# Kernel tuning notes

Hardware: AMD Instinct MI355X
Metric: run time of the kernel (lower is better)

## Reference

```python
import jax, jax.numpy as jnp
import numpy as np

N_NODES = 50000
N_EDGES = 800000
NUM_FEATURES = 3
HIDDEN = 128
NUM_GRAPHS = 100
NUM_CLASSES = 2


def setup_inputs() -> dict:
    key = jax.random.key(0)
    ks = jax.random.split(key, 12)
    x = jax.random.normal(ks[0], (N_NODES, NUM_FEATURES), dtype=jnp.float32)
    edge_index = jax.random.randint(ks[1], (2, N_EDGES), 0, N_NODES, dtype=jnp.int64)
    batch = jnp.sort(jax.random.randint(ks[2], (N_NODES,), 0, NUM_GRAPHS, dtype=jnp.int64))
    c1, c2, c3 = 4 * HIDDEN, 2 * HIDDEN, HIDDEN  # 512, 256, 128

    def glorot(k, fan_in, fan_out):
        s = jnp.sqrt(6.0 / (fan_in + fan_out)).astype(jnp.float32)
        return jax.random.uniform(k, (fan_in, fan_out), jnp.float32, -s, s)

    W1 = glorot(ks[3], NUM_FEATURES, c1); b1 = jnp.zeros((c1,), jnp.float32)
    W2 = glorot(ks[4], c1, c2);           b2 = jnp.zeros((c2,), jnp.float32)
    W3 = glorot(ks[5], c2, c3);           b3 = jnp.zeros((c3,), jnp.float32)
    Wc = glorot(ks[6], c3, NUM_CLASSES);  bc = jnp.zeros((NUM_CLASSES,), jnp.float32)
    return {"x": x, "W1": W1, "b1": b1, "W2": W2, "b2": b2, "W3": W3, "b3": b3,
            "Wc": Wc, "bc": bc, "edge_index": edge_index, "batch": batch}


def reference(x, W1, b1, W2, b2, W3, b3, Wc, bc, edge_index, batch):
    n = x.shape[0]
    self_loop = jnp.arange(n, dtype=edge_index.dtype)
    row = jnp.concatenate([edge_index[0], self_loop])  # source nodes (messages from)
    col = jnp.concatenate([edge_index[1], self_loop])  # target nodes (aggregate into)
    # symmetric GCN normalization with self-loops: deg^{-1/2}[row] * deg^{-1/2}[col]
    deg = jax.ops.segment_sum(jnp.ones(row.shape, x.dtype), col, num_segments=n)
    dis = jnp.where(deg > 0, jax.lax.rsqrt(jnp.maximum(deg, 1.0)), 0.0)
    norm = dis[row] * dis[col]  # [E + N]

    def gcn_conv(h, W, b):
        m = h @ W                                   # project first (cheap GEMM)
        agg = jax.ops.segment_sum(norm[:, None] * m[row], col, num_segments=n)
        return agg + b

    h = jax.nn.relu(gcn_conv(x, W1, b1))
    h = jax.nn.relu(gcn_conv(h, W2, b2))
    h = jax.nn.relu(gcn_conv(h, W3, b3))

    # global mean pool over graphs
    counts = jax.ops.segment_sum(jnp.ones((n,), h.dtype), batch, num_segments=NUM_GRAPHS)
    pooled = jax.ops.segment_sum(h, batch, num_segments=NUM_GRAPHS) / jnp.maximum(counts, 1.0)[:, None]

    logits = pooled @ Wc + bc
    return jax.nn.log_softmax(logits, axis=1)
```

## Files before the change

kernel.cpp:

```cpp
#include <hip/hip_runtime.h>
#include <hip/hip_bf16.h>
#include <hip/hip_fp8.h>
#include <math.h>

#define N_NODES 50000
#define N_EDGES 800000
#define NFEAT 3
#define C1 512
#define C2 256
#define C3 128
#define NGRAPH 100
#define NCLS 2
#define PSPLIT 8
#define NRANGE 8
#define RANGE_SZ 6250

typedef short bh8 __attribute__((ext_vector_type(8)));
typedef float f32x4 __attribute__((ext_vector_type(4)));

__device__ __forceinline__ short f2bf(float x) {
    __hip_bfloat16 h = __float2bfloat16(x);
    return *reinterpret_cast<short*>(&h);
}
__device__ __forceinline__ float bflo(unsigned int u) { return __uint_as_float(u << 16); }
__device__ __forceinline__ float bfhi(unsigned int u) { return __uint_as_float(u & 0xffff0000u); }
__device__ __forceinline__ unsigned int packbf(float a, float b) {
    return (unsigned int)(unsigned short)f2bf(a) | ((unsigned int)(unsigned short)f2bf(b) << 16);
}
__device__ __forceinline__ unsigned char f2fp8(float x) {
    __hip_fp8_e4m3 q(x);
    return (unsigned char)q.__x;
}
__device__ __forceinline__ float2 fp8x2(unsigned short u) {
    __hip_fp8x2_e4m3 q; q.__x = u; return (float2)q;
}


__global__ void count_edges(const int* __restrict__ col, int* __restrict__ counts) {
    int range = blockIdx.x & (NRANGE - 1);
    int e = (blockIdx.x >> 3) * 256 + threadIdx.x;
    if (e < N_EDGES) {
        int c = col[e];
        int lo = range * RANGE_SZ;
        if (c >= lo && c < lo + RANGE_SZ) atomicAdd(&counts[c], 1);
    }
}


__global__ void scan_chunks(const int* __restrict__ counts, const float* __restrict__ x,
                            int* __restrict__ offsets, int* __restrict__ chunksums,
                            float* __restrict__ dis, float4* __restrict__ xd) {
    __shared__ int s[256];
    int b = blockIdx.x, t = threadIdx.x;
    int i = b * 256 + t;
    int v = (i < N_NODES) ? counts[i] : 0;
    if (i < N_NODES) {
        float d = rsqrtf((float)(v + 1));
        dis[i] = d;
        xd[i] = make_float4(x[i * 3 + 0], x[i * 3 + 1], x[i * 3 + 2], d);
    }
    s[t] = v;
    __syncthreads();
    for (int d = 1; d < 256; d <<= 1) {
        int add = (t >= d) ? s[t - d] : 0;
        __syncthreads();
        s[t] += add;
        __syncthreads();
    }
    if (i < N_NODES) offsets[i + 1] = s[t];
    if (t == 255) chunksums[b] = s[255];
}

__global__ void scan_sums(int* __restrict__ chunksums, int nchunks) {
    __shared__ int s[256];
    int t = threadIdx.x;
    int v = (t < nchunks) ? chunksums[t] : 0;
    s[t] = v;
    __syncthreads();
    for (int d = 1; d < 256; d <<= 1) {
        int add = (t >= d) ? s[t - d] : 0;
        __syncthreads();
        s[t] += add;
        __syncthreads();
    }
    if (t < nchunks) chunksums[t] = (t == 0) ? 0 : s[t - 1];
}

__global__ void finalize_offsets(int* __restrict__ offsets, const int* __restrict__ chunkoffs,
                                 int* __restrict__ cursor) {
    int i = blockIdx.x * blockDim.x + threadIdx.x;
    if (i < N_NODES) {
        int v = offsets[i + 1] + chunkoffs[i / 256];
        offsets[i + 1] = v;
        if (i + 1 < N_NODES) cursor[i + 1] = v;
    }
    if (i == 0) { offsets[0] = 0; cursor[0] = 0; }
}

__global__ void scatter_edges(const int* __restrict__ rowi, const int* __restrict__ coli,
                              int* __restrict__ cursor, int* __restrict__ csr_src) {
    int range = blockIdx.x & (NRANGE - 1);
    int e = (blockIdx.x >> 3) * 256 + threadIdx.x;
    if (e < N_EDGES) {
        int c = coli[e];
        int lo = range * RANGE_SZ;
        if (c >= lo && c < lo + RANGE_SZ) {
            int p = atomicAdd(&cursor[c], 1);
            csr_src[p] = rowi[e];
        }
    }
}


__global__ void prep_weights(const float* __restrict__ W2, const float* __restrict__ W3,
                             short* __restrict__ W2t, short* __restrict__ W3t) {
    int idx = blockIdx.x * 256 + threadIdx.x;
    if (idx < C1 * C2) {
        int n = idx / C1, k = idx % C1;
        W2t[idx] = f2bf(W2[k * C2 + n]);
    } else if (idx < C1 * C2 + C2 * C3) {
        int j = idx - C1 * C2;
        int n = j / C2, k = j % C2;
        W3t[j] = f2bf(W3[k * C3 + n]);
    }
}


__global__ __launch_bounds__(256) void agg_feat3(const float4* __restrict__ xd,
                                                 const int* __restrict__ offsets,
                                                 const int* __restrict__ csr_src,
                                                 float* __restrict__ aggx) {
    int t = threadIdx.x;
    int l = t & 15;
    int i = blockIdx.x * 16 + (t >> 4);
    if (i >= N_NODES) return;
    int s = offsets[i], e = offsets[i + 1];
    float a0 = 0.f, a1 = 0.f, a2 = 0.f;
    for (int p = s + l; p < e; p += 16) {
        int r = csr_src[p];
        float4 v = xd[r];
        a0 += v.w * v.x;
        a1 += v.w * v.y;
        a2 += v.w * v.z;
    }
#pragma unroll
    for (int m = 1; m < 16; m <<= 1) {
        a0 += __shfl_xor(a0, m);
        a1 += __shfl_xor(a1, m);
        a2 += __shfl_xor(a2, m);
    }
    if (l == 0) {
        float4 self = xd[i];
        float di = self.w;
        a0 += di * self.x; a1 += di * self.y; a2 += di * self.z;
        aggx[i * 3 + 0] = di * a0;
        aggx[i * 3 + 1] = di * a1;
        aggx[i * 3 + 2] = di * a2;
    }
}


__global__ __launch_bounds__(512, 4) void gemm_l1(const float* __restrict__ aggx,
                                                  const float* __restrict__ W1,
                                                  const float* __restrict__ b1,
                                                  const float* __restrict__ dis,
                                                  const short* __restrict__ Bt,
                                                  unsigned char* __restrict__ Cmat, int M) {
    __shared__ short As[128 * 32];
    __shared__ short Bs[C2 * 32];
    __shared__ float sW1[3 * C1];
    __shared__ float sb1[C1];
    __shared__ float sa[128 * 3];
    __shared__ float sd[128];
    int bm = blockIdx.x * 128;
    int t = threadIdx.x;
    int wave = t >> 6, lane = t & 63, quad = lane >> 4, l16 = lane & 15;
    int wm = (wave >> 2) * 64;
    int wn = (wave & 3) * 64;
    f32x4 acc[4][4] = {};

    for (int j = t; j < 3 * C1; j += 512) sW1[j] = W1[j];
    if (t < C1) sb1[t] = b1[t];
    if (t < 128 * 3) {
        int r = bm + t / 3; if (r > M - 1) r = M - 1;
        sa[t] = aggx[r * 3 + (t % 3)];
    }
    if (t < 128) {
        int r = bm + t; if (r > M - 1) r = M - 1;
        sd[t] = dis[r];
    }
    __syncthreads();

    int ar = t >> 2, ak = (t & 3) * 8;
    int br = t >> 1, bk = (t & 1) * 16;
    float a0 = sa[ar * 3 + 0], a1 = sa[ar * 3 + 1], a2 = sa[ar * 3 + 2];
    float drow = sd[ar];

    for (int k0 = 0; k0 < C1; k0 += 32) {
#pragma unroll
        for (int j = 0; j < 8; ++j) {
            int k = k0 + ak + j;
            float v = a0 * sW1[k] + a1 * sW1[C1 + k] + a2 * sW1[2 * C1 + k] + sb1[k];
            As[ar * 32 + ak + j] = f2bf(drow * fmaxf(v, 0.f));
        }
        const short* bptr = Bt + (size_t)br * C1 + bk + k0;
        *(bh8*)&Bs[br * 32 + bk]     = *(const bh8*)bptr;
        *(bh8*)&Bs[br * 32 + bk + 8] = *(const bh8*)(bptr + 8);
        __syncthreads();
        bh8 af[4], bf[4];
#pragma unroll
        for (int mt = 0; mt < 4; ++mt)
            af[mt] = *(const bh8*)&As[(wm + mt * 16 + l16) * 32 + quad * 8];
#pragma unroll
        for (int nt = 0; nt < 4; ++nt)
            bf[nt] = *(const bh8*)&Bs[(wn + nt * 16 + l16) * 32 + quad * 8];
#pragma unroll
        for (int mt = 0; mt < 4; ++mt)
#pragma unroll
            for (int nt = 0; nt < 4; ++nt)
                acc[mt][nt] = __builtin_amdgcn_mfma_f32_16x16x32_bf16(af[mt], bf[nt], acc[mt][nt], 0, 0, 0);
        __syncthreads();
    }

#pragma unroll
    for (int mt = 0; mt < 4; ++mt)
#pragma unroll
        for (int nt = 0; nt < 4; ++nt) {
            int colc = wn + nt * 16 + l16;
#pragma unroll
            for (int r = 0; r < 4; ++r) {
                int rowc = bm + wm + mt * 16 + quad * 4 + r;
                if (rowc < M) Cmat[(size_t)rowc * C2 + colc] = f2fp8(acc[mt][nt][r]);
            }
        }
}


template <int K, int BN>
__global__ __launch_bounds__(512, 4) void gemm_bf16(const short* __restrict__ A,
                                                    const short* __restrict__ Bt,
                                                    unsigned char* __restrict__ Cmat, int M) {
    __shared__ short As[128 * 32];
    __shared__ short Bs[BN * 32];
    constexpr int NT = BN / 64;
    int bm = blockIdx.x * 128;
    int t = threadIdx.x;
    int wave = t >> 6, lane = t & 63, quad = lane >> 4, l16 = lane & 15;
    int wm = (wave >> 2) * 64;
    int wn = (wave & 3) * (BN / 4);
    f32x4 acc[4][NT] = {};

    int ar = t >> 2, ak = (t & 3) * 8;
    int agr = bm + ar; if (agr > M - 1) agr = M - 1;
    const short* aptr = A + (size_t)agr * K + ak;

    for (int k0 = 0; k0 < K; k0 += 32) {
        *(bh8*)&As[ar * 32 + ak] = *(const bh8*)(aptr + k0);
        if constexpr (BN == 256) {
            int br = t >> 1, bk = (t & 1) * 16;
            const short* bptr = Bt + (size_t)br * K + bk + k0;
            *(bh8*)&Bs[br * 32 + bk]     = *(const bh8*)bptr;
            *(bh8*)&Bs[br * 32 + bk + 8] = *(const bh8*)(bptr + 8);
        } else {
            int br = t >> 2, bk = (t & 3) * 8;
            *(bh8*)&Bs[br * 32 + bk] = *(const bh8*)(Bt + (size_t)br * K + bk + k0);
        }
        __syncthreads();
        bh8 af[4], bf[NT];
#pragma unroll
        for (int mt = 0; mt < 4; ++mt)
            af[mt] = *(const bh8*)&As[(wm + mt * 16 + l16) * 32 + quad * 8];
#pragma unroll
        for (int nt = 0; nt < NT; ++nt)
            bf[nt] = *(const bh8*)&Bs[(wn + nt * 16 + l16) * 32 + quad * 8];
#pragma unroll
        for (int mt = 0; mt < 4; ++mt)
#pragma unroll
            for (int nt = 0; nt < NT; ++nt)
                acc[mt][nt] = __builtin_amdgcn_mfma_f32_16x16x32_bf16(af[mt], bf[nt], acc[mt][nt], 0, 0, 0);
        __syncthreads();
    }

#pragma unroll
    for (int mt = 0; mt < 4; ++mt)
#pragma unroll
        for (int nt = 0; nt < NT; ++nt) {
            int colc = wn + nt * 16 + l16;
#pragma unroll
            for (int r = 0; r < 4; ++r) {
                int rowc = bm + wm + mt * 16 + quad * 4 + r;
                if (rowc < M) Cmat[(size_t)rowc * BN + colc] = f2fp8(acc[mt][nt][r]);
            }
        }
}


template <int C, bool PRESCALE>
__global__ __launch_bounds__(256) void aggregate_w(const unsigned char* __restrict__ m,
                                                   const int* __restrict__ offsets,
                                                   const int* __restrict__ csr_src,
                                                   const float* __restrict__ dis,
                                                   const float* __restrict__ bias,
                                                   short* __restrict__ out) {
    int i = blockIdx.x * 4 + (threadIdx.x >> 6);
    if (i >= N_NODES) return;
    int lane = threadIdx.x & 63;
    int s = __builtin_amdgcn_readfirstlane(offsets[i]);
    int e = __builtin_amdgcn_readfirstlane(offsets[i + 1]);
    float di = __uint_as_float(__builtin_amdgcn_readfirstlane(__float_as_uint(dis[i])));

    if constexpr (C == 256) {
        const unsigned int* mu = (const unsigned int*)m;
        unsigned int su = mu[(size_t)i * (C / 4) + lane];
        float2 slo = fp8x2((unsigned short)(su & 0xffffu));
        float2 shi = fp8x2((unsigned short)(su >> 16));
        float a0 = slo.x, a1 = slo.y, a2 = shi.x, a3 = shi.y;
        int p = s;
        for (; p + 16 <= e; p += 16) {
            unsigned int u[16];
#pragma unroll
            for (int j = 0; j < 16; ++j) {
                int r = csr_src[p + j];
                u[j] = mu[(size_t)r * (C / 4) + lane];
            }
#pragma unroll
            for (int j = 0; j < 16; ++j) {
                float2 lo = fp8x2((unsigned short)(u[j] & 0xffffu));
                float2 hi = fp8x2((unsigned short)(u[j] >> 16));
                a0 += lo.x; a1 += lo.y; a2 += hi.x; a3 += hi.y;
            }
        }
        if (p < e) {
            unsigned int u[16];
            float sc[16];
#pragma unroll
            for (int j = 0; j < 16; ++j) {
                int q = p + j;
                sc[j] = (q < e) ? 1.f : 0.f;
                int r = csr_src[(q < e) ? q : e - 1];
                u[j] = mu[(size_t)r * (C / 4) + lane];
            }
#pragma unroll
            for (int j = 0; j < 16; ++j) {
                float2 lo = fp8x2((unsigned short)(u[j] & 0xffffu));
                float2 hi = fp8x2((unsigned short)(u[j] >> 16));
                a0 = fmaf(sc[j], lo.x, a0);
                a1 = fmaf(sc[j], lo.y, a1);
                a2 = fmaf(sc[j], hi.x, a2);
                a3 = fmaf(sc[j], hi.y, a3);
            }
        }
        float4 b = *(const float4*)&bias[4 * lane];
        a0 = fmaxf(di * a0 + b.x, 0.f);
        a1 = fmaxf(di * a1 + b.y, 0.f);
        a2 = fmaxf(di * a2 + b.z, 0.f);
        a3 = fmaxf(di * a3 + b.w, 0.f);
        if (PRESCALE) { a0 *= di; a1 *= di; a2 *= di; a3 *= di; }
        uint2 o;
        o.x = packbf(a0, a1);
        o.y = packbf(a2, a3);
        *(uint2*)(out + (size_t)i * C + 4 * lane) = o;
    } else {
        const unsigned short* mu = (const unsigned short*)m;
        float2 sf = fp8x2(mu[(size_t)i * (C / 2) + lane]);
        float a0 = sf.x, a1 = sf.y;
        int p = s;
        for (; p + 16 <= e; p += 16) {
            unsigned short u[16];
#pragma unroll
            for (int j = 0; j < 16; ++j) {
                int r = csr_src[p + j];
                u[j] = mu[(size_t)r * (C / 2) + lane];
            }
#pragma unroll
            for (int j = 0; j < 16; ++j) {
                float2 f = fp8x2(u[j]);
                a0 += f.x; a1 += f.y;
            }
        }
        if (p < e) {
            unsigned short u[16];
            float sc[16];
#pragma unroll
            for (int j = 0; j < 16; ++j) {
                int q = p + j;
                sc[j] = (q < e) ? 1.f : 0.f;
                int r = csr_src[(q < e) ? q : e - 1];
                u[j] = mu[(size_t)r * (C / 2) + lane];
            }
#pragma unroll
            for (int j = 0; j < 16; ++j) {
                float2 f = fp8x2(u[j]);
                a0 = fmaf(sc[j], f.x, a0);
                a1 = fmaf(sc[j], f.y, a1);
            }
        }
        float2 b = *(const float2*)&bias[2 * lane];
        a0 = fmaxf(di * a0 + b.x, 0.f);
        a1 = fmaxf(di * a1 + b.y, 0.f);
        if (PRESCALE) { a0 *= di; a1 *= di; }
        ((unsigned int*)out)[(size_t)i * (C / 2) + lane] = packbf(a0, a1);
    }
}


__global__ void pool_partial(const short* __restrict__ h3, const int* __restrict__ batch,
                             float* __restrict__ pooled) {
    int g = blockIdx.x, sp = blockIdx.y;
    int t = threadIdx.x;
    __shared__ int seg[2];
    if (t < 2) {
        int target = g + t;
        int lo = 0, hi = N_NODES;
        while (lo < hi) { int mid = (lo + hi) >> 1; if (batch[mid] < target) lo = mid + 1; else hi = mid; }
        seg[t] = lo;
    }
    __syncthreads();
    int start = seg[0], end = seg[1];
    int len = end - start;
    int chunk = (len + PSPLIT - 1) / PSPLIT;
    int a = start + sp * chunk;
    int b = a + chunk; if (b > end) b = end;
    if (a >= b) return;
    const unsigned int* hu = (const unsigned int*)h3;
    float s0 = 0.f, s1 = 0.f;
    int i = a;
    for (; i + 4 <= b; i += 4) {
        unsigned int u0 = hu[(size_t)(i + 0) * (C3 / 2) + t];
        unsigned int u1 = hu[(size_t)(i + 1) * (C3 / 2) + t];
        unsigned int u2 = hu[(size_t)(i + 2) * (C3 / 2) + t];
        unsigned int u3 = hu[(size_t)(i + 3) * (C3 / 2) + t];
        s0 += bflo(u0) + bflo(u1) + bflo(u2) + bflo(u3);
        s1 += bfhi(u0) + bfhi(u1) + bfhi(u2) + bfhi(u3);
    }
    for (; i < b; ++i) {
        unsigned int u = hu[(size_t)i * (C3 / 2) + t];
        s0 += bflo(u);
        s1 += bfhi(u);
    }
    atomicAdd(&pooled[g * C3 + 2 * t], s0);
    atomicAdd(&pooled[g * C3 + 2 * t + 1], s1);
}


__global__ void finalize_head(const float* __restrict__ pooled, const int* __restrict__ batch,
                              const float* __restrict__ Wc, const float* __restrict__ bc,
                              float* __restrict__ outp) {
    int g = blockIdx.x;
    int t = threadIdx.x;
    __shared__ int seg[2];
    if (t < 2) {
        int target = g + t;
        int lo = 0, hi = N_NODES;
        while (lo < hi) { int mid = (lo + hi) >> 1; if (batch[mid] < target) lo = mid + 1; else hi = mid; }
        seg[t] = lo;
    }
    __syncthreads();
    float cnt = (float)(seg[1] - seg[0]);
    float pv = pooled[(size_t)g * C3 + t] / fmaxf(cnt, 1.f);
    float p0 = pv * Wc[t * 2 + 0];
    float p1 = pv * Wc[t * 2 + 1];
#pragma unroll
    for (int o = 32; o > 0; o >>= 1) {
        p0 += __shfl_down(p0, o);
        p1 += __shfl_down(p1, o);
    }
    __shared__ float r0[2], r1[2];
    int wid = t >> 6, lane = t & 63;
    if (lane == 0) { r0[wid] = p0; r1[wid] = p1; }
    __syncthreads();
    if (t == 0) {
        float l0 = r0[0] + r0[1] + bc[0];
        float l1 = r1[0] + r1[1] + bc[1];
        float mx = fmaxf(l0, l1);
        float lse = mx + logf(expf(l0 - mx) + expf(l1 - mx));
        outp[g * 2 + 0] = l0 - lse;
        outp[g * 2 + 1] = l1 - lse;
    }
}


extern "C" void kernel_launch(void* const* d_in, const int* in_sizes, int n_in,
                              void* d_out, int out_size, void* d_ws, size_t ws_size,
                              hipStream_t stream) {
    const float* x = (const float*)d_in[0];
    const float* W1 = (const float*)d_in[1];
    const float* b1 = (const float*)d_in[2];
    const float* W2 = (const float*)d_in[3];
    const float* b2 = (const float*)d_in[4];
    const float* W3 = (const float*)d_in[5];
    const float* b3 = (const float*)d_in[6];
    const float* Wc = (const float*)d_in[7];
    const float* bc = (const float*)d_in[8];
    const int* ei = (const int*)d_in[9];
    const int* batch = (const int*)d_in[10];
    const int* row = ei;
    const int* col = ei + N_EDGES;
    float* out = (float*)d_out;

    char* ws = (char*)d_ws;
    size_t off = 0;
    auto alloc = [&](size_t bytes) -> void* {
        off = (off + 255) & ~(size_t)255;
        void* p = ws + off;
        off += bytes;
        return p;
    };

    int* counts = (int*)alloc((size_t)N_NODES * 4);
    int* offsets = (int*)alloc((size_t)(N_NODES + 1) * 4);
    int* cursor = (int*)alloc((size_t)N_NODES * 4);
    int* chunksums = (int*)alloc(256 * 4);
    float* dis = (float*)alloc((size_t)N_NODES * 4);
    float4* xd = (float4*)alloc((size_t)N_NODES * 16);
    int* csr_src = (int*)alloc((size_t)N_EDGES * 4);
    float* aggx = (float*)alloc((size_t)N_NODES * 3 * 4);
    short* W2t = (short*)alloc((size_t)C1 * C2 * 2);
    short* W3t = (short*)alloc((size_t)C2 * C3 * 2);
    unsigned char* m2 = (unsigned char*)alloc((size_t)N_NODES * C2);
    short* h2 = (short*)alloc((size_t)N_NODES * C2 * 2);
    unsigned char* m3 = (unsigned char*)alloc((size_t)N_NODES * C3);
    short* h3 = (short*)alloc((size_t)N_NODES * C3 * 2);
    float* pooled = (float*)alloc((size_t)NGRAPH * C3 * 4);

    hipMemsetAsync(counts, 0, (size_t)N_NODES * 4, stream);
    hipMemsetAsync(pooled, 0, (size_t)NGRAPH * C3 * 4, stream);
    int nechunks = (N_EDGES + 255) / 256;
    count_edges<<<nechunks * NRANGE, 256, 0, stream>>>(col, counts);
    int nchunks = (N_NODES + 255) / 256;
    scan_chunks<<<nchunks, 256, 0, stream>>>(counts, x, offsets, chunksums, dis, xd);
    scan_sums<<<1, 256, 0, stream>>>(chunksums, nchunks);
    finalize_offsets<<<(N_NODES + 255) / 256, 256, 0, stream>>>(offsets, chunksums, cursor);
    scatter_edges<<<nechunks * NRANGE, 256, 0, stream>>>(row, col, cursor, csr_src);

    prep_weights<<<(C1 * C2 + C2 * C3 + 255) / 256, 256, 0, stream>>>(W2, W3, W2t, W3t);

    agg_feat3<<<(N_NODES + 15) / 16, 256, 0, stream>>>(xd, offsets, csr_src, aggx);

    gemm_l1<<<(N_NODES + 127) / 128, 512, 0, stream>>>(aggx, W1, b1, dis, W2t, m2, N_NODES);
    aggregate_w<C2, true><<<(N_NODES + 3) / 4, 256, 0, stream>>>(m2, offsets, csr_src, dis, b2, h2);

    gemm_bf16<C2, C3><<<(N_NODES + 127) / 128, 512, 0, stream>>>(h2, W3t, m3, N_NODES);
    aggregate_w<C3, false><<<(N_NODES + 3) / 4, 256, 0, stream>>>(m3, offsets, csr_src, dis, b3, h3);

    dim3 gp(NGRAPH, PSPLIT);
    pool_partial<<<gp, C3 / 2, 0, stream>>>(h3, batch, pooled);
    finalize_head<<<NGRAPH, C3, 0, stream>>>(pooled, batch, Wc, bc, out);
}
```

Baseline: 282.9 us.

## Fuse small kernels: weight prep into counting, feature aggregation into GEMM, pooling into aggregation

Merges the weight transpose and cast into the edge-counting launch, and folds the chunk-sum scan into finalize_offsets. The layer-1 three-feature aggregation now runs inside gemm_l1, and the last aggregation pushes results straight into the pooled buffer with atomics. This drops several launches and the aggx and h3 intermediate buffers, and two memsets are merged into one. In exchange, every finalize_offsets block redoes the small scan, gemm_l1 blocks do irregular gathers before their GEMM, and global float atomics per node add contention and make the summation order nondeterministic.

```diff
diff --git a/kernel.cpp b/kernel.cpp
--- a/kernel.cpp
+++ b/kernel.cpp
@@ -11,9 +11,10 @@
 #define C3 128
 #define NGRAPH 100
 #define NCLS 2
-#define PSPLIT 8
 #define NRANGE 8
 #define RANGE_SZ 6250
+#define NECHUNK 3125
+#define WBLK 640
 
 typedef short bh8 __attribute__((ext_vector_type(8)));
 typedef float f32x4 __attribute__((ext_vector_type(4)));
@@ -22,8 +23,6 @@
     __hip_bfloat16 h = __float2bfloat16(x);
     return *reinterpret_cast<short*>(&h);
 }
-__device__ __forceinline__ float bflo(unsigned int u) { return __uint_as_float(u << 16); }
-__device__ __forceinline__ float bfhi(unsigned int u) { return __uint_as_float(u & 0xffff0000u); }
 __device__ __forceinline__ unsigned int packbf(float a, float b) {
     return (unsigned int)(unsigned short)f2bf(a) | ((unsigned int)(unsigned short)f2bf(b) << 16);
 }
@@ -36,13 +35,28 @@
 }
 
 
-__global__ void count_edges(const int* __restrict__ col, int* __restrict__ counts) {
-    int range = blockIdx.x & (NRANGE - 1);
-    int e = (blockIdx.x >> 3) * 256 + threadIdx.x;
-    if (e < N_EDGES) {
-        int c = col[e];
-        int lo = range * RANGE_SZ;
-        if (c >= lo && c < lo + RANGE_SZ) atomicAdd(&counts[c], 1);
+__global__ void count_prep(const int* __restrict__ col, int* __restrict__ counts,
+                           const float* __restrict__ W2, const float* __restrict__ W3,
+                           short* __restrict__ W2t, short* __restrict__ W3t) {
+    int b = blockIdx.x;
+    if (b < NECHUNK * NRANGE) {
+        int range = b & (NRANGE - 1);
+        int e = (b >> 3) * 256 + threadIdx.x;
+        if (e < N_EDGES) {
+            int c = col[e];
+            int lo = range * RANGE_SZ;
+            if (c >= lo && c < lo + RANGE_SZ) atomicAdd(&counts[c], 1);
+        }
+    } else {
+        int idx = (b - NECHUNK * NRANGE) * 256 + threadIdx.x;
+        if (idx < C1 * C2) {
+            int n = idx / C1, k = idx % C1;
+            W2t[idx] = f2bf(W2[k * C2 + n]);
+        } else if (idx < C1 * C2 + C2 * C3) {
+            int j = idx - C1 * C2;
+            int n = j / C2, k = j % C2;
+            W3t[j] = f2bf(W3[k * C3 + n]);
+        }
     }
 }
 
@@ -71,11 +85,13 @@
     if (t == 255) chunksums[b] = s[255];
 }
 
-__global__ void scan_sums(int* __restrict__ chunksums, int nchunks) {
+
+__global__ void finalize_offsets(int* __restrict__ offsets, const int* __restrict__ chunksums,
+                                 int* __restrict__ cursor) {
     __shared__ int s[256];
-    int t = threadIdx.x;
-    int v = (t < nchunks) ? chunksums[t] : 0;
-    s[t] = v;
+    int b = blockIdx.x, t = threadIdx.x;
+    int nck = (N_NODES + 255) / 256;
+    s[t] = (t < nck) ? chunksums[t] : 0;
     __syncthreads();
     for (int d = 1; d < 256; d <<= 1) {
         int add = (t >= d) ? s[t - d] : 0;
@@ -83,16 +99,12 @@
         s[t] += add;
         __syncthreads();
     }
-    if (t < nchunks) chunksums[t] = (t == 0) ? 0 : s[t - 1];
-}
-
-__global__ void finalize_offsets(int* __restrict__ offsets, const int* __restrict__ chunkoffs,
-                                 int* __restrict__ cursor) {
-    int i = blockIdx.x * blockDim.x + threadIdx.x;
+    int add = (b == 0) ? 0 : s[b - 1];
+    int i = b * 256 + t;
     if (i < N_NODES) {
-        int v = offsets[i + 1] + chunkoffs[i / 256];
-        offsets[i + 1] = v;
-        if (i + 1 < N_NODES) cursor[i + 1] = v;
+        int val = offsets[i + 1] + add;
+        offsets[i + 1] = val;
+        if (i + 1 < N_NODES) cursor[i + 1] = val;
     }
     if (i == 0) { offsets[0] = 0; cursor[0] = 0; }
 }
@@ -112,58 +124,11 @@
 }
 
 
-__global__ void prep_weights(const float* __restrict__ W2, const float* __restrict__ W3,
-                             short* __restrict__ W2t, short* __restrict__ W3t) {
-    int idx = blockIdx.x * 256 + threadIdx.x;
-    if (idx < C1 * C2) {
-        int n = idx / C1, k = idx % C1;
-        W2t[idx] = f2bf(W2[k * C2 + n]);
-    } else if (idx < C1 * C2 + C2 * C3) {
-        int j = idx - C1 * C2;
-        int n = j / C2, k = j % C2;
-        W3t[j] = f2bf(W3[k * C3 + n]);
-    }
-}
-
-
-__global__ __launch_bounds__(256) void agg_feat3(const float4* __restrict__ xd,
-                                                 const int* __restrict__ offsets,
-                                                 const int* __restrict__ csr_src,
-                                                 float* __restrict__ aggx) {
-    int t = threadIdx.x;
-    int l = t & 15;
-    int i = blockIdx.x * 16 + (t >> 4);
-    if (i >= N_NODES) return;
-    int s = offsets[i], e = offsets[i + 1];
-    float a0 = 0.f, a1 = 0.f, a2 = 0.f;
-    for (int p = s + l; p < e; p += 16) {
-        int r = csr_src[p];
-        float4 v = xd[r];
-        a0 += v.w * v.x;
-        a1 += v.w * v.y;
-        a2 += v.w * v.z;
-    }
-#pragma unroll
-    for (int m = 1; m < 16; m <<= 1) {
-        a0 += __shfl_xor(a0, m);
-        a1 += __shfl_xor(a1, m);
-        a2 += __shfl_xor(a2, m);
-    }
-    if (l == 0) {
-        float4 self = xd[i];
-        float di = self.w;
-        a0 += di * self.x; a1 += di * self.y; a2 += di * self.z;
-        aggx[i * 3 + 0] = di * a0;
-        aggx[i * 3 + 1] = di * a1;
-        aggx[i * 3 + 2] = di * a2;
-    }
-}
-
-
-__global__ __launch_bounds__(512, 4) void gemm_l1(const float* __restrict__ aggx,
+__global__ __launch_bounds__(512, 4) void gemm_l1(const float4* __restrict__ xd,
+                                                  const int* __restrict__ offsets,
+                                                  const int* __restrict__ csr_src,
                                                   const float* __restrict__ W1,
                                                   const float* __restrict__ b1,
-                                                  const float* __restrict__ dis,
                                                   const short* __restrict__ Bt,
                                                   unsigned char* __restrict__ Cmat, int M) {
     __shared__ short As[128 * 32];
@@ -181,13 +146,36 @@
 
     for (int j = t; j < 3 * C1; j += 512) sW1[j] = W1[j];
     if (t < C1) sb1[t] = b1[t];
-    if (t < 128 * 3) {
-        int r = bm + t / 3; if (r > M - 1) r = M - 1;
-        sa[t] = aggx[r * 3 + (t % 3)];
-    }
-    if (t < 128) {
-        int r = bm + t; if (r > M - 1) r = M - 1;
-        sd[t] = dis[r];
+
+    int lg = t & 15;
+#pragma unroll
+    for (int rnd = 0; rnd < 4; ++rnd) {
+        int rloc = rnd * 32 + (t >> 4);
+        int i = bm + rloc; if (i > M - 1) i = M - 1;
+        int s0 = offsets[i], e0 = offsets[i + 1];
+        float a0 = 0.f, a1 = 0.f, a2 = 0.f;
+        for (int p = s0 + lg; p < e0; p += 16) {
+            int r = csr_src[p];
+            float4 v = xd[r];
+            a0 += v.w * v.x;
+            a1 += v.w * v.y;
+            a2 += v.w * v.z;
+        }
+#pragma unroll
+        for (int m = 1; m < 16; m <<= 1) {
+            a0 += __shfl_xor(a0, m);
+            a1 += __shfl_xor(a1, m);
+            a2 += __shfl_xor(a2, m);
+        }
+        if (lg == 0) {
+            float4 self = xd[i];
+            float di = self.w;
+            a0 += di * self.x; a1 += di * self.y; a2 += di * self.z;
+            sa[rloc * 3 + 0] = di * a0;
+            sa[rloc * 3 + 1] = di * a1;
+            sa[rloc * 3 + 2] = di * a2;
+            sd[rloc] = di;
+        }
     }
     __syncthreads();
 
@@ -309,137 +297,113 @@
     int e = __builtin_amdgcn_readfirstlane(offsets[i + 1]);
     float di = __uint_as_float(__builtin_amdgcn_readfirstlane(__float_as_uint(dis[i])));
 
-    if constexpr (C == 256) {
-        const unsigned int* mu = (const unsigned int*)m;
-        unsigned int su = mu[(size_t)i * (C / 4) + lane];
-        float2 slo = fp8x2((unsigned short)(su & 0xffffu));
-        float2 shi = fp8x2((unsigned short)(su >> 16));
-        float a0 = slo.x, a1 = slo.y, a2 = shi.x, a3 = shi.y;
-        int p = s;
-        for (; p + 16 <= e; p += 16) {
-            unsigned int u[16];
-#pragma unroll
-            for (int j = 0; j < 16; ++j) {
-                int r = csr_src[p + j];
-                u[j] = mu[(size_t)r * (C / 4) + lane];
-            }
-#pragma unroll
-            for (int j = 0; j < 16; ++j) {
-                float2 lo = fp8x2((unsigned short)(u[j] & 0xffffu));
-                float2 hi = fp8x2((unsigned short)(u[j] >> 16));
-                a0 += lo.x; a1 += lo.y; a2 += hi.x; a3 += hi.y;
-            }
-        }
-        if (p < e) {
-            unsigned int u[16];
-            float sc[16];
-#pragma unroll
-            for (int j = 0; j < 16; ++j) {
-                int q = p + j;
-                sc[j] = (q < e) ? 1.f : 0.f;
-                int r = csr_src[(q < e) ? q : e - 1];
-                u[j] = mu[(size_t)r * (C / 4) + lane];
-            }
-#pragma unroll
-            for (int j = 0; j < 16; ++j) {
-                float2 lo = fp8x2((unsigned short)(u[j] & 0xffffu));
-                float2 hi = fp8x2((unsigned short)(u[j] >> 16));
-                a0 = fmaf(sc[j], lo.x, a0);
-                a1 = fmaf(sc[j], lo.y, a1);
-                a2 = fmaf(sc[j], hi.x, a2);
-                a3 = fmaf(sc[j], hi.y, a3);
-            }
-        }
-        float4 b = *(const float4*)&bias[4 * lane];
-        a0 = fmaxf(di * a0 + b.x, 0.f);
-        a1 = fmaxf(di * a1 + b.y, 0.f);
-        a2 = fmaxf(di * a2 + b.z, 0.f);
-        a3 = fmaxf(di * a3 + b.w, 0.f);
-        if (PRESCALE) { a0 *= di; a1 *= di; a2 *= di; a3 *= di; }
-        uint2 o;
-        o.x = packbf(a0, a1);
-        o.y = packbf(a2, a3);
-        *(uint2*)(out + (size_t)i * C + 4 * lane) = o;
-    } else {
-        const unsigned short* mu = (const unsigned short*)m;
-        float2 sf = fp8x2(mu[(size_t)i * (C / 2) + lane]);
-        float a0 = sf.x, a1 = sf.y;
-        int p = s;
-        for (; p + 16 <= e; p += 16) {
-            unsigned short u[16];
-#pragma unroll
-            for (int j = 0; j < 16; ++j) {
-                int r = csr_src[p + j];
-                u[j] = mu[(size_t)r * (C / 2) + lane];
-            }
-#pragma unroll
-            for (int j = 0; j < 16; ++j) {
-                float2 f = fp8x2(u[j]);
-                a0 += f.x; a1 += f.y;
-            }
-        }
-        if (p < e) {
-            unsigned short u[16];
-            float sc[16];
-#pragma unroll
-            for (int j = 0; j < 16; ++j) {
-                int q = p + j;
-                sc[j] = (q < e) ? 1.f : 0.f;
-                int r = csr_src[(q < e) ? q : e - 1];
-                u[j] = mu[(size_t)r * (C / 2) + lane];
-            }
-#pragma unroll
-            for (int j = 0; j < 16; ++j) {
-                float2 f = fp8x2(u[j]);
-                a0 = fmaf(sc[j], f.x, a0);
-                a1 = fmaf(sc[j], f.y, a1);
-            }
-        }
-        float2 b = *(const float2*)&bias[2 * lane];
-        a0 = fmaxf(di * a0 + b.x, 0.f);
-        a1 = fmaxf(di * a1 + b.y, 0.f);
-        if (PRESCALE) { a0 *= di; a1 *= di; }
-        ((unsigned int*)out)[(size_t)i * (C / 2) + lane] = packbf(a0, a1);
-    }
-}
-
-
-__global__ void pool_partial(const short* __restrict__ h3, const int* __restrict__ batch,
-                             float* __restrict__ pooled) {
-    int g = blockIdx.x, sp = blockIdx.y;
-    int t = threadIdx.x;
-    __shared__ int seg[2];
-    if (t < 2) {
-        int target = g + t;
-        int lo = 0, hi = N_NODES;
-        while (lo < hi) { int mid = (lo + hi) >> 1; if (batch[mid] < target) lo = mid + 1; else hi = mid; }
-        seg[t] = lo;
-    }
-    __syncthreads();
-    int start = seg[0], end = seg[1];
-    int len = end - start;
-    int chunk = (len + PSPLIT - 1) / PSPLIT;
-    int a = start + sp * chunk;
-    int b = a + chunk; if (b > end) b = end;
-    if (a >= b) return;
-    const unsigned int* hu = (const unsigned int*)h3;
-    float s0 = 0.f, s1 = 0.f;
-    int i = a;
-    for (; i + 4 <= b; i += 4) {
-        unsigned int u0 = hu[(size_t)(i + 0) * (C3 / 2) + t];
-        unsigned int u1 = hu[(size_t)(i + 1) * (C3 / 2) + t];
-        unsigned int u2 = hu[(size_t)(i + 2) * (C3 / 2) + t];
-        unsigned int u3 = hu[(size_t)(i + 3) * (C3 / 2) + t];
-        s0 += bflo(u0) + bflo(u1) + bflo(u2) + bflo(u3);
-        s1 += bfhi(u0) + bfhi(u1) + bfhi(u2) + bfhi(u3);
-    }
-    for (; i < b; ++i) {
-        unsigned int u = hu[(size_t)i * (C3 / 2) + t];
-        s0 += bflo(u);
-        s1 += bfhi(u);
-    }
-    atomicAdd(&pooled[g * C3 + 2 * t], s0);
-    atomicAdd(&pooled[g * C3 + 2 * t + 1], s1);
+    const unsigned int* mu = (const unsigned int*)m;
+    unsigned int su = mu[(size_t)i * (C / 4) + lane];
+    float2 slo = fp8x2((unsigned short)(su & 0xffffu));
+    float2 shi = fp8x2((unsigned short)(su >> 16));
+    float a0 = slo.x, a1 = slo.y, a2 = shi.x, a3 = shi.y;
+    int p = s;
+    for (; p + 16 <= e; p += 16) {
+        unsigned int u[16];
+#pragma unroll
+        for (int j = 0; j < 16; ++j) {
+            int r = csr_src[p + j];
+            u[j] = mu[(size_t)r * (C / 4) + lane];
+        }
+#pragma unroll
+        for (int j = 0; j < 16; ++j) {
+            float2 lo = fp8x2((unsigned short)(u[j] & 0xffffu));
+            float2 hi = fp8x2((unsigned short)(u[j] >> 16));
+            a0 += lo.x; a1 += lo.y; a2 += hi.x; a3 += hi.y;
+        }
+    }
+    if (p < e) {
+        unsigned int u[16];
+        float sc[16];
+#pragma unroll
+        for (int j = 0; j < 16; ++j) {
+            int q = p + j;
+            sc[j] = (q < e) ? 1.f : 0.f;
+            int r = csr_src[(q < e) ? q : e - 1];
+            u[j] = mu[(size_t)r * (C / 4) + lane];
+        }
+#pragma unroll
+        for (int j = 0; j < 16; ++j) {
+            float2 lo = fp8x2((unsigned short)(u[j] & 0xffffu));
+            float2 hi = fp8x2((unsigned short)(u[j] >> 16));
+            a0 = fmaf(sc[j], lo.x, a0);
+            a1 = fmaf(sc[j], lo.y, a1);
+            a2 = fmaf(sc[j], hi.x, a2);
+            a3 = fmaf(sc[j], hi.y, a3);
+        }
+    }
+    float4 b = *(const float4*)&bias[4 * lane];
+    a0 = fmaxf(di * a0 + b.x, 0.f);
+    a1 = fmaxf(di * a1 + b.y, 0.f);
+    a2 = fmaxf(di * a2 + b.z, 0.f);
+    a3 = fmaxf(di * a3 + b.w, 0.f);
+    if (PRESCALE) { a0 *= di; a1 *= di; a2 *= di; a3 *= di; }
+    uint2 o;
+    o.x = packbf(a0, a1);
+    o.y = packbf(a2, a3);
+    *(uint2*)(out + (size_t)i * C + 4 * lane) = o;
+}
+
+
+__global__ __launch_bounds__(256) void aggregate_pool(const unsigned char* __restrict__ m,
+                                                      const int* __restrict__ offsets,
+                                                      const int* __restrict__ csr_src,
+                                                      const float* __restrict__ dis,
+                                                      const float* __restrict__ bias,
+                                                      const int* __restrict__ batch,
+                                                      float* __restrict__ pooled) {
+    int i = blockIdx.x * 4 + (threadIdx.x >> 6);
+    if (i >= N_NODES) return;
+    int lane = threadIdx.x & 63;
+    int s = __builtin_amdgcn_readfirstlane(offsets[i]);
+    int e = __builtin_amdgcn_readfirstlane(offsets[i + 1]);
+    float di = __uint_as_float(__builtin_amdgcn_readfirstlane(__float_as_uint(dis[i])));
+
+    const unsigned short* mu = (const unsigned short*)m;
+    float2 sf = fp8x2(mu[(size_t)i * (C3 / 2) + lane]);
+    float a0 = sf.x, a1 = sf.y;
+    int p = s;
+    for (; p + 16 <= e; p += 16) {
+        unsigned short u[16];
+#pragma unroll
+        for (int j = 0; j < 16; ++j) {
+            int r = csr_src[p + j];
+            u[j] = mu[(size_t)r * (C3 / 2) + lane];
+        }
+#pragma unroll
+        for (int j = 0; j < 16; ++j) {
+            float2 f = fp8x2(u[j]);
+            a0 += f.x; a1 += f.y;
+        }
+    }
+    if (p < e) {
+        unsigned short u[16];
+        float sc[16];
+#pragma unroll
+        for (int j = 0; j < 16; ++j) {
+            int q = p + j;
+            sc[j] = (q < e) ? 1.f : 0.f;
+            int r = csr_src[(q < e) ? q : e - 1];
+            u[j] = mu[(size_t)r * (C3 / 2) + lane];
+        }
+#pragma unroll
+        for (int j = 0; j < 16; ++j) {
+            float2 f = fp8x2(u[j]);
+            a0 = fmaf(sc[j], f.x, a0);
+            a1 = fmaf(sc[j], f.y, a1);
+        }
+    }
+    float2 b = *(const float2*)&bias[2 * lane];
+    a0 = fmaxf(di * a0 + b.x, 0.f);
+    a1 = fmaxf(di * a1 + b.y, 0.f);
+    int g = __builtin_amdgcn_readfirstlane(batch[i]);
+    atomicAdd(&pooled[(size_t)g * C3 + 2 * lane], a0);
+    atomicAdd(&pooled[(size_t)g * C3 + 2 * lane + 1], a1);
 }
 
 
@@ -508,42 +472,34 @@
     };
 
     int* counts = (int*)alloc((size_t)N_NODES * 4);
+    float* pooled = (float*)alloc((size_t)NGRAPH * C3 * 4);
+    size_t zero_bytes = off;
+
     int* offsets = (int*)alloc((size_t)(N_NODES + 1) * 4);
     int* cursor = (int*)alloc((size_t)N_NODES * 4);
     int* chunksums = (int*)alloc(256 * 4);
     float* dis = (float*)alloc((size_t)N_NODES * 4);
     float4* xd = (float4*)alloc((size_t)N_NODES * 16);
     int* csr_src = (int*)alloc((size_t)N_EDGES * 4);
-    float* aggx = (float*)alloc((size_t)N_NODES * 3 * 4);
     short* W2t = (short*)alloc((size_t)C1 * C2 * 2);
     short* W3t = (short*)alloc((size_t)C2 * C3 * 2);
     unsigned char* m2 = (unsigned char*)alloc((size_t)N_NODES * C2);
     short* h2 = (short*)alloc((size_t)N_NODES * C2 * 2);
     unsigned char* m3 = (unsigned char*)alloc((size_t)N_NODES * C3);
-    short* h3 = (short*)alloc((size_t)N_NODES * C3 * 2);
-    float* pooled = (float*)alloc((size_t)NGRAPH * C3 * 4);
-
-    hipMemsetAsync(counts, 0, (size_t)N_NODES * 4, stream);
-    hipMemsetAsync(pooled, 0, (size_t)NGRAPH * C3 * 4, stream);
-    int nechunks = (N_EDGES + 255) / 256;
-    count_edges<<<nechunks * NRANGE, 256, 0, stream>>>(col, counts);
+
+    hipMemsetAsync(ws, 0, zero_bytes, stream);
+
+    count_prep<<<NECHUNK * NRANGE + WBLK, 256, 0, stream>>>(col, counts, W2, W3, W2t, W3t);
     int nchunks = (N_NODES + 255) / 256;
     scan_chunks<<<nchunks, 256, 0, stream>>>(counts, x, offsets, chunksums, dis, xd);
-    scan_sums<<<1, 256, 0, stream>>>(chunksums, nchunks);
-    finalize_offsets<<<(N_NODES + 255) / 256, 256, 0, stream>>>(offsets, chunksums, cursor);
-    scatter_edges<<<nechunks * NRANGE, 256, 0, stream>>>(row, col, cursor, csr_src);
-
-    prep_weights<<<(C1 * C2 + C2 * C3 + 255) / 256, 256, 0, stream>>>(W2, W3, W2t, W3t);
-
-    agg_feat3<<<(N_NODES + 15) / 16, 256, 0, stream>>>(xd, offsets, csr_src, aggx);
-
-    gemm_l1<<<(N_NODES + 127) / 128, 512, 0, stream>>>(aggx, W1, b1, dis, W2t, m2, N_NODES);
+    finalize_offsets<<<nchunks, 256, 0, stream>>>(offsets, chunksums, cursor);
+    scatter_edges<<<NECHUNK * NRANGE, 256, 0, stream>>>(row, col, cursor, csr_src);
+
+    gemm_l1<<<(N_NODES + 127) / 128, 512, 0, stream>>>(xd, offsets, csr_src, W1, b1, W2t, m2, N_NODES);
     aggregate_w<C2, true><<<(N_NODES + 3) / 4, 256, 0, stream>>>(m2, offsets, csr_src, dis, b2, h2);
 
     gemm_bf16<C2, C3><<<(N_NODES + 127) / 128, 512, 0, stream>>>(h2, W3t, m3, N_NODES);
-    aggregate_w<C3, false><<<(N_NODES + 3) / 4, 256, 0, stream>>>(m3, offsets, csr_src, dis, b3, h3);
-
-    dim3 gp(NGRAPH, PSPLIT);
-    pool_partial<<<gp, C3 / 2, 0, stream>>>(h3, batch, pooled);
+    aggregate_pool<<<(N_NODES + 3) / 4, 256, 0, stream>>>(m3, offsets, csr_src, dis, b3, batch, pooled);
+
     finalize_head<<<NGRAPH, C3, 0, stream>>>(pooled, batch, Wc, bc, out);
 }
```

Result: slower. 356.6 us (+26.1%).
